# Performance work log

Hardware: AMD Instinct MI355X
Metric: run time of the kernel (lower is better)

## Reference

```python
import jax, jax.numpy as jnp
import numpy as np

DIM = 768
HEADS = 12
HEAD_DIM = DIM // HEADS
SCALE = HEAD_DIM ** (-0.5)


def setup_inputs() -> dict:
    key = jax.random.key(0)
    k1, k2, k3 = jax.random.split(key, 3)
    x = jax.random.normal(k1, (4, 2048, DIM), dtype=jnp.float32)
    # nn.Linear(dim, 3*dim, bias=False): weight [3*dim, dim]
    w_qkv = jax.random.normal(k2, (3 * DIM, DIM), dtype=jnp.float32) * (DIM ** -0.5)
    # nn.Linear(dim, dim) with bias
    w_proj = jax.random.normal(k3, (DIM, DIM), dtype=jnp.float32) * (DIM ** -0.5)
    b_proj = jnp.zeros((DIM,), dtype=jnp.float32)
    return {"x": x, "w_qkv": w_qkv, "w_proj": w_proj, "b_proj": b_proj}


def reference(x, w_qkv, w_proj, b_proj):
    B, N, C = x.shape
    H, D = HEADS, HEAD_DIM
    qkv = jnp.einsum('bnc,oc->bno', x, w_qkv)  # [B,N,3C]
    qkv = qkv.reshape(B, N, 3, H, D).transpose(2, 0, 3, 1, 4)  # [3,B,H,N,D]
    q, k, v = qkv[0], qkv[1], qkv[2]
    attn = jnp.einsum('bhnd,bhmd->bhnm', q, k) * SCALE  # [B,H,N,N]
    attn = jax.nn.softmax(attn, axis=-1)
    attn = jax.nn.softmax(attn, axis=-1)  # double softmax, as in original
    out = jnp.einsum('bhnm,bhmd->bhnd', attn, v)  # [B,H,N,D]
    out = out.transpose(0, 2, 1, 3).reshape(B, N, C)
    return jnp.einsum('bnc,oc->bno', out, w_proj) + b_proj
```

## Files before the change

kernel.cpp:

```cpp
#include <hip/hip_runtime.h>
#include <hip/hip_bf16.h>

#define DIM 768
#define HEADS 12
#define HD 64
#define SEQ 2048
#define BATCH 4
#define BHN 48
#define TOK 8192

#if __has_builtin(__builtin_amdgcn_exp2f)
#define EXP2F __builtin_amdgcn_exp2f
#else
#define EXP2F exp2f
#endif
#define EXP_C 0.1803368801111244f

using short8  = __attribute__((ext_vector_type(8))) short;
using float4v = __attribute__((ext_vector_type(4))) float;

__device__ __forceinline__ short f2b(float f) {
    union { float f; unsigned u; } v; v.f = f;
    unsigned r = v.u + 0x7FFF + ((v.u >> 16) & 1);
    return (short)(r >> 16);
}
__device__ __forceinline__ float b2f(short s) {
    union { unsigned u; float f; } v;
    v.u = ((unsigned)(unsigned short)s) << 16;
    return v.f;
}
__device__ __forceinline__ unsigned pk2(float a, float b) {
    union { float f; unsigned u; } x, y; x.f = a; y.f = b;
    return ((x.u + 0x8000u) >> 16) | ((y.u + 0x8000u) & 0xFFFF0000u);
}

typedef const __attribute__((address_space(1))) unsigned GU;
typedef __attribute__((address_space(3))) unsigned LU;
__device__ __forceinline__ void gload_lds16(const short* g, short* l) {
    __builtin_amdgcn_global_load_lds((GU*)g, (LU*)l, 16, 0, 0);
}

__global__ void cast_all(const float* __restrict__ x, const float* __restrict__ wq,
                         const float* __restrict__ wp,
                         short* __restrict__ xb, short* __restrict__ wqb,
                         short* __restrict__ wpb, int nx4, int nq4) {
    int i = blockIdx.x * 256 + threadIdx.x;
    const float* in; short* out; int j = i;
    if (i < nx4)            { in = x;  out = xb;  }
    else if (i < nx4 + nq4) { in = wq; out = wqb; j = i - nx4; }
    else                    { in = wp; out = wpb; j = i - nx4 - nq4; }
    float4 f = ((const float4*)in)[j];
    short4 o;
    o.x = f2b(f.x); o.y = f2b(f.y); o.z = f2b(f.z); o.w = f2b(f.w);
    ((short4*)out)[j] = o;
}

__global__ void vsum_kernel(const short* __restrict__ Vw, float* __restrict__ Vsum) {
    int wid  = blockIdx.x * 4 + (threadIdx.x >> 6);
    int lane = threadIdx.x & 63;
    const short* row = Vw + (size_t)wid * SEQ;
    float s = 0.f;
    for (int i = lane; i < SEQ; i += 64) s += b2f(row[i]);
    #pragma unroll
    for (int m = 1; m < 64; m <<= 1) s += __shfl_xor(s, m, 64);
    if (lane == 0) Vsum[wid] = s;
}

template<int MODE>
__global__ __launch_bounds__(256, 4)
void gemm_bt(const short* __restrict__ A, const short* __restrict__ Bw,
             const float* __restrict__ bias,
             short* __restrict__ Qw, short* __restrict__ Kw, short* __restrict__ Vw,
             float* __restrict__ Out, int K)
{
    __shared__ __align__(16) short As[128 * 32];
    __shared__ __align__(16) short Bs[128 * 32];

    const int tid  = threadIdx.x;
    const int lane = tid & 63;
    const int wave = tid >> 6;
    const int wm = (wave >> 1) * 64, wn = (wave & 1) * 64;
    const int l15 = lane & 15, quad = lane >> 4;

    const bool vpart = (MODE == 0) && (blockIdx.x >= 12);
    const short* rowsP = vpart ? (Bw + 1536 * 768) : A;
    const short* colsP = vpart ? A : Bw;
    const int m0 = vpart ? (blockIdx.x - 12) * 128 : blockIdx.y * 128;
    const int n0 = vpart ? blockIdx.y * 128 : blockIdx.x * 128;

    float4v acc[4][4];
    #pragma unroll
    for (int i = 0; i < 4; i++)
        #pragma unroll
        for (int j = 0; j < 4; j++)
            acc[i][j] = (float4v){0.f, 0.f, 0.f, 0.f};

    const int G0 = wave * 128 + lane;
    const int G1 = G0 + 64;
    const int rA0 = G0 >> 2, cA0 = (G0 & 3) * 8;
    const int rA1 = G1 >> 2, cA1 = (G1 & 3) * 8;
    short* ldsA0 = &As[(wave * 128) * 8];
    short* ldsA1 = &As[(wave * 128 + 64) * 8];
    short* ldsB0 = &Bs[(wave * 128) * 8];
    short* ldsB1 = &Bs[(wave * 128 + 64) * 8];

    for (int kt = 0; kt < K; kt += 32) {
        gload_lds16(&rowsP[(size_t)(m0 + rA0) * K + kt + cA0], ldsA0);
        gload_lds16(&rowsP[(size_t)(m0 + rA1) * K + kt + cA1], ldsA1);
        gload_lds16(&colsP[(size_t)(n0 + rA0) * K + kt + cA0], ldsB0);
        gload_lds16(&colsP[(size_t)(n0 + rA1) * K + kt + cA1], ldsB1);
        __syncthreads();
        short8 af[4], bfr[4];
        #pragma unroll
        for (int t = 0; t < 4; t++) {
            af[t]  = *(const short8*)&As[(wm + t * 16 + l15) * 32 + quad * 8];
            bfr[t] = *(const short8*)&Bs[(wn + t * 16 + l15) * 32 + quad * 8];
        }
        #pragma unroll
        for (int tm = 0; tm < 4; tm++)
            #pragma unroll
            for (int tn = 0; tn < 4; tn++)
                acc[tm][tn] = __builtin_amdgcn_mfma_f32_16x16x32_bf16(af[tm], bfr[tn], acc[tm][tn], 0, 0, 0);
        __syncthreads();
    }

    #pragma unroll
    for (int tm = 0; tm < 4; tm++)
        #pragma unroll
        for (int tn = 0; tn < 4; tn++)
            #pragma unroll
            for (int r = 0; r < 4; r++) {
                int row = m0 + wm + tm * 16 + quad * 4 + r;
                int col = n0 + wn + tn * 16 + l15;
                float v = acc[tm][tn][r];
                if (MODE == 0) {
                    if (vpart) {
                        int hh = row >> 6, d = row & 63;
                        int b = col >> 11, n = col & 2047;
                        Vw[((size_t)(b * HEADS + hh) * 64 + d) * SEQ + n] = f2b(v);
                    } else {
                        int hh = (col & 767) >> 6, d = col & 63;
                        int b = row >> 11, n = row & 2047;
                        int bh = b * HEADS + hh;
                        if (col < 768) Qw[((size_t)bh * SEQ + n) * 64 + d] = f2b(v * EXP_C);
                        else           Kw[((size_t)bh * SEQ + n) * 64 + d] = f2b(v);
                    }
                } else {
                    Out[(size_t)row * 768 + col] = v + bias[col];
                }
            }
}

__global__ __launch_bounds__(256, 3)
void attn_kernel(const short* __restrict__ Qw, const short* __restrict__ Kw,
                 const short* __restrict__ Vw, const float* __restrict__ Vsum,
                 short* __restrict__ Ow)
{
    __shared__ __align__(16) short KE[128 * 72];
    __shared__ __align__(16) short Eb[64 * 136];
    __shared__ __align__(16) short Vt[64 * 136];

    const int tid  = threadIdx.x;
    const int lane = tid & 63, wave = tid >> 6;
    const int l15 = lane & 15, quad = lane >> 4;
    const int bh = blockIdx.x >> 5;
    const int n0 = (blockIdx.x & 31) * 64;
    const int wq = (wave & 2) * 16;
    const int wk = (wave & 1) * 64;

    const short* Qp = Qw + (size_t)bh * SEQ * 64;
    const short* Kp = Kw + (size_t)bh * SEQ * 64;
    const short* Vp = Vw + (size_t)bh * 64 * SEQ;

    short8 onesf;
    #pragma unroll
    for (int j = 0; j < 8; j++) onesf[j] = (l15 == 0) ? (short)0x3F80 : (short)0;

    #pragma unroll
    for (int h = 0; h < 2; h++) {
        int c = tid + h * 256;
        int row = c >> 3, cc = (c & 7) * 8;
        *(short8*)&Eb[row * 72 + cc] = *(const short8*)&Qp[(size_t)(n0 + row) * 64 + cc];
    }
    __syncthreads();
    short8 aq[2][2];
    #pragma unroll
    for (int nb = 0; nb < 2; nb++)
        #pragma unroll
        for (int kk = 0; kk < 2; kk++)
            aq[nb][kk] = *(const short8*)&Eb[(wq + nb * 16 + l15) * 72 + kk * 32 + quad * 8];

    float4v Aacc[2][4], Lacc[2];
    #pragma unroll
    for (int mb = 0; mb < 2; mb++) {
        Lacc[mb] = (float4v){0.f, 0.f, 0.f, 0.f};
        #pragma unroll
        for (int t = 0; t < 4; t++) Aacc[mb][t] = (float4v){0.f, 0.f, 0.f, 0.f};
    }

    short8 kr[4], vr[4];
    #pragma unroll
    for (int h = 0; h < 4; h++) {
        int c = tid + h * 256;
        int row = c >> 3, cc = (c & 7) * 8;
        kr[h] = *(const short8*)&Kp[(size_t)row * 64 + cc];
        int vrow = c >> 4, vc = (c & 15) * 8;
        vr[h] = *(const short8*)&Vp[(size_t)vrow * SEQ + vc];
    }

    for (int kt = 0; kt < 16; kt++) {
        __syncthreads();
        #pragma unroll
        for (int h = 0; h < 4; h++) {
            int c = tid + h * 256;
            int row = c >> 3, cc = (c & 7) * 8;
            *(short8*)&KE[row * 72 + cc] = kr[h];
            int vrow = c >> 4, vc = (c & 15) * 8;
            *(short8*)&Vt[vrow * 136 + vc] = vr[h];
        }
        __syncthreads();

        if (kt < 15) {
            #pragma unroll
            for (int h = 0; h < 4; h++) {
                int c = tid + h * 256;
                int row = c >> 3, cc = (c & 7) * 8;
                kr[h] = *(const short8*)&Kp[(size_t)((kt + 1) * 128 + row) * 64 + cc];
                int vrow = c >> 4, vc = (c & 15) * 8;
                vr[h] = *(const short8*)&Vp[(size_t)vrow * SEQ + (kt + 1) * 128 + vc];
            }
        }

        float4v sacc[2][4];
        #pragma unroll
        for (int nb = 0; nb < 2; nb++)
            #pragma unroll
            for (int tn = 0; tn < 4; tn++) sacc[nb][tn] = (float4v){0.f, 0.f, 0.f, 0.f};
        #pragma unroll
        for (int tn = 0; tn < 4; tn++) {
            const int rowK = (wk + tn * 16 + l15) * 72;
            short8 b0 = *(const short8*)&KE[rowK + quad * 8];
            short8 b1 = *(const short8*)&KE[rowK + 32 + quad * 8];
            #pragma unroll
            for (int nb = 0; nb < 2; nb++) {
                sacc[nb][tn] = __builtin_amdgcn_mfma_f32_16x16x32_bf16(b0, aq[nb][0], sacc[nb][tn], 0, 0, 0);
                sacc[nb][tn] = __builtin_amdgcn_mfma_f32_16x16x32_bf16(b1, aq[nb][1], sacc[nb][tn], 0, 0, 0);
            }
        }

        #pragma unroll
        for (int nb = 0; nb < 2; nb++) {
            const int qrow = (wq + nb * 16 + l15) * 136;
            #pragma unroll
            for (int tn = 0; tn < 4; tn++) {
                float e0 = EXP2F(sacc[nb][tn][0]);
                float e1 = EXP2F(sacc[nb][tn][1]);
                float e2 = EXP2F(sacc[nb][tn][2]);
                float e3 = EXP2F(sacc[nb][tn][3]);
                uint2 u; u.x = pk2(e0, e1); u.y = pk2(e2, e3);
                *(uint2*)&Eb[qrow + wk + tn * 16 + quad * 4] = u;
            }
        }

        #pragma unroll
        for (int ks = 0; ks < 2; ks++) {
            const int koff = wk + ks * 32 + quad * 8;
            short8 ae0 = *(const short8*)&Eb[(wq + l15) * 136 + koff];
            short8 ae1 = *(const short8*)&Eb[(wq + 16 + l15) * 136 + koff];
            Lacc[0] = __builtin_amdgcn_mfma_f32_16x16x32_bf16(ae0, onesf, Lacc[0], 0, 0, 0);
            Lacc[1] = __builtin_amdgcn_mfma_f32_16x16x32_bf16(ae1, onesf, Lacc[1], 0, 0, 0);
            #pragma unroll
            for (int tn = 0; tn < 4; tn++) {
                short8 bv = *(const short8*)&Vt[(tn * 16 + l15) * 136 + koff];
                Aacc[0][tn] = __builtin_amdgcn_mfma_f32_16x16x32_bf16(ae0, bv, Aacc[0][tn], 0, 0, 0);
                Aacc[1][tn] = __builtin_amdgcn_mfma_f32_16x16x32_bf16(ae1, bv, Aacc[1][tn], 0, 0, 0);
            }
        }
    }

    __syncthreads();
    float* KEf = (float*)KE;
    float* Vtf = (float*)Vt;
    const int p = wave >> 1;
    if (wave & 1) {
        #pragma unroll
        for (int mb = 0; mb < 2; mb++) {
            #pragma unroll
            for (int tn = 0; tn < 4; tn++)
                #pragma unroll
                for (int r = 0; r < 4; r++)
                    KEf[(mb * 16 + tn * 4 + r) * 128 + p * 64 + lane] = Aacc[mb][tn][r];
            #pragma unroll
            for (int r = 0; r < 4; r++)
                Vtf[(mb * 4 + r) * 128 + p * 64 + lane] = Lacc[mb][r];
        }
    }
    __syncthreads();
    if (!(wave & 1)) {
        float il[2][4];
        #pragma unroll
        for (int mb = 0; mb < 2; mb++)
            #pragma unroll
            for (int r = 0; r < 4; r++) {
                float ls = Lacc[mb][r] + Vtf[(mb * 4 + r) * 128 + p * 64 + lane];
                il[mb][r] = 1.f / __shfl(ls, lane & 48, 64);
            }
        const int b = bh / HEADS, hh = bh - (bh / HEADS) * HEADS;
        #pragma unroll
        for (int tn = 0; tn < 4; tn++) {
            int d = tn * 16 + l15;
            float vs = Vsum[bh * 64 + d];
            #pragma unroll
            for (int mb = 0; mb < 2; mb++)
                #pragma unroll
                for (int r = 0; r < 4; r++) {
                    float a = Aacc[mb][tn][r] + KEf[(mb * 16 + tn * 4 + r) * 128 + p * 64 + lane];
                    int row = n0 + wq + mb * 16 + quad * 4 + r;
                    float val = (vs + a * il[mb][r]) * (1.f / 2049.f);
                    int tok = b * SEQ + row;
                    Ow[(size_t)tok * 768 + hh * 64 + d] = f2b(val);
                }
        }
    }
}

extern "C" void kernel_launch(void* const* d_in, const int* in_sizes, int n_in,
                              void* d_out, int out_size, void* d_ws, size_t ws_size,
                              hipStream_t stream) {
    const float* x      = (const float*)d_in[0];
    const float* w_qkv  = (const float*)d_in[1];
    const float* w_proj = (const float*)d_in[2];
    const float* b_proj = (const float*)d_in[3];
    float* out = (float*)d_out;

    char* ws = (char*)d_ws;
    size_t off = 0;
    auto alloc = [&](size_t bytes) {
        void* p = ws + off;
        off += (bytes + 255) & ~(size_t)255;
        return p;
    };
    short* x_bf  = (short*)alloc((size_t)TOK * DIM * 2);
    short* wq_bf = (short*)alloc((size_t)3 * DIM * DIM * 2);
    short* wp_bf = (short*)alloc((size_t)DIM * DIM * 2);
    short* Qw    = (short*)alloc((size_t)BHN * SEQ * 64 * 2);
    short* Kw    = (short*)alloc((size_t)BHN * SEQ * 64 * 2);
    short* Vw    = (short*)alloc((size_t)BHN * SEQ * 64 * 2);
    short* Ow    = (short*)alloc((size_t)TOK * DIM * 2);
    float* Vsum  = (float*)alloc((size_t)BHN * 64 * 4);

    int nx4 = TOK * DIM / 4, nq4 = 3 * DIM * DIM / 4, np4 = DIM * DIM / 4;
    int tot4 = nx4 + nq4 + np4;
    cast_all<<<tot4 / 256, 256, 0, stream>>>(x, w_qkv, w_proj, x_bf, wq_bf, wp_bf, nx4, nq4);

    dim3 g1(18, TOK / 128);
    gemm_bt<0><<<g1, 256, 0, stream>>>(x_bf, wq_bf, nullptr, Qw, Kw, Vw, nullptr, DIM);

    vsum_kernel<<<BHN * 64 / 4, 256, 0, stream>>>(Vw, Vsum);

    attn_kernel<<<BHN * 32, 256, 0, stream>>>(Qw, Kw, Vw, Vsum, Ow);

    dim3 g3(DIM / 128, TOK / 128);
    gemm_bt<1><<<g3, 256, 0, stream>>>(Ow, wp_bf, b_proj, nullptr, nullptr, nullptr, out, DIM);
}
```

Before: 243.2 us.

## Split GEMM into QKV and projection kernels with grouped block order and K=64 stages

The templated GEMM becomes two kernels. Each one now loads two 32-wide K slices per barrier pair, which halves the number of __syncthreads calls, and maps a 1D grid through grouped swizzling so neighbouring blocks share A/B tiles in L2. The projection GEMM switches to 128x64 tiles, giving 768 blocks instead of 384 so the GPU's CUs are filled better. The cost is twice the LDS per block, which may limit occupancy, and still no overlap of the loads with the MFMA work.

Result: faster. 226.0 us (-7.1%).

```diff
diff --git a/kernel.cpp b/kernel.cpp
--- a/kernel.cpp
+++ b/kernel.cpp
@@ -66,15 +66,12 @@
     if (lane == 0) Vsum[wid] = s;
 }
 
-template<int MODE>
 __global__ __launch_bounds__(256, 4)
-void gemm_bt(const short* __restrict__ A, const short* __restrict__ Bw,
-             const float* __restrict__ bias,
-             short* __restrict__ Qw, short* __restrict__ Kw, short* __restrict__ Vw,
-             float* __restrict__ Out, int K)
+void gemm_qkv(const short* __restrict__ A, const short* __restrict__ Bw,
+              short* __restrict__ Qw, short* __restrict__ Kw, short* __restrict__ Vw)
 {
-    __shared__ __align__(16) short As[128 * 32];
-    __shared__ __align__(16) short Bs[128 * 32];
+    __shared__ __align__(16) short As[2][128 * 32];
+    __shared__ __align__(16) short Bs[2][128 * 32];
 
     const int tid  = threadIdx.x;
     const int lane = tid & 63;
@@ -82,11 +79,17 @@
     const int wm = (wave >> 1) * 64, wn = (wave & 1) * 64;
     const int l15 = lane & 15, quad = lane >> 4;
 
-    const bool vpart = (MODE == 0) && (blockIdx.x >= 12);
+    const int gid = blockIdx.x;
+    const int w   = gid >> 3;
+    const int ybl = (gid & 7) * 8 + (w & 7);
+    const int xbl = w >> 3;
+
+    const bool vpart = (xbl >= 12);
     const short* rowsP = vpart ? (Bw + 1536 * 768) : A;
     const short* colsP = vpart ? A : Bw;
-    const int m0 = vpart ? (blockIdx.x - 12) * 128 : blockIdx.y * 128;
-    const int n0 = vpart ? blockIdx.y * 128 : blockIdx.x * 128;
+    const int m0 = vpart ? (xbl - 12) * 128 : ybl * 128;
+    const int n0 = vpart ? ybl * 128 : xbl * 128;
+    const int K = DIM;
 
     float4v acc[4][4];
     #pragma unroll
@@ -99,28 +102,32 @@
     const int G1 = G0 + 64;
     const int rA0 = G0 >> 2, cA0 = (G0 & 3) * 8;
     const int rA1 = G1 >> 2, cA1 = (G1 & 3) * 8;
-    short* ldsA0 = &As[(wave * 128) * 8];
-    short* ldsA1 = &As[(wave * 128 + 64) * 8];
-    short* ldsB0 = &Bs[(wave * 128) * 8];
-    short* ldsB1 = &Bs[(wave * 128 + 64) * 8];
-
-    for (int kt = 0; kt < K; kt += 32) {
-        gload_lds16(&rowsP[(size_t)(m0 + rA0) * K + kt + cA0], ldsA0);
-        gload_lds16(&rowsP[(size_t)(m0 + rA1) * K + kt + cA1], ldsA1);
-        gload_lds16(&colsP[(size_t)(n0 + rA0) * K + kt + cA0], ldsB0);
-        gload_lds16(&colsP[(size_t)(n0 + rA1) * K + kt + cA1], ldsB1);
-        __syncthreads();
-        short8 af[4], bfr[4];
-        #pragma unroll
-        for (int t = 0; t < 4; t++) {
-            af[t]  = *(const short8*)&As[(wm + t * 16 + l15) * 32 + quad * 8];
-            bfr[t] = *(const short8*)&Bs[(wn + t * 16 + l15) * 32 + quad * 8];
-        }
-        #pragma unroll
-        for (int tm = 0; tm < 4; tm++)
-            #pragma unroll
-            for (int tn = 0; tn < 4; tn++)
-                acc[tm][tn] = __builtin_amdgcn_mfma_f32_16x16x32_bf16(af[tm], bfr[tn], acc[tm][tn], 0, 0, 0);
+    const int ldsoff = wave * 1024;
+
+    for (int kt = 0; kt < K; kt += 64) {
+        #pragma unroll
+        for (int s = 0; s < 2; s++) {
+            const int kc = kt + s * 32;
+            gload_lds16(&rowsP[(size_t)(m0 + rA0) * K + kc + cA0], &As[s][ldsoff]);
+            gload_lds16(&rowsP[(size_t)(m0 + rA1) * K + kc + cA1], &As[s][ldsoff + 512]);
+            gload_lds16(&colsP[(size_t)(n0 + rA0) * K + kc + cA0], &Bs[s][ldsoff]);
+            gload_lds16(&colsP[(size_t)(n0 + rA1) * K + kc + cA1], &Bs[s][ldsoff + 512]);
+        }
+        __syncthreads();
+        #pragma unroll
+        for (int s = 0; s < 2; s++) {
+            short8 af[4], bfr[4];
+            #pragma unroll
+            for (int t = 0; t < 4; t++) {
+                af[t]  = *(const short8*)&As[s][(wm + t * 16 + l15) * 32 + quad * 8];
+                bfr[t] = *(const short8*)&Bs[s][(wn + t * 16 + l15) * 32 + quad * 8];
+            }
+            #pragma unroll
+            for (int tm = 0; tm < 4; tm++)
+                #pragma unroll
+                for (int tn = 0; tn < 4; tn++)
+                    acc[tm][tn] = __builtin_amdgcn_mfma_f32_16x16x32_bf16(af[tm], bfr[tn], acc[tm][tn], 0, 0, 0);
+        }
         __syncthreads();
     }
 
@@ -133,21 +140,90 @@
                 int row = m0 + wm + tm * 16 + quad * 4 + r;
                 int col = n0 + wn + tn * 16 + l15;
                 float v = acc[tm][tn][r];
-                if (MODE == 0) {
-                    if (vpart) {
-                        int hh = row >> 6, d = row & 63;
-                        int b = col >> 11, n = col & 2047;
-                        Vw[((size_t)(b * HEADS + hh) * 64 + d) * SEQ + n] = f2b(v);
-                    } else {
-                        int hh = (col & 767) >> 6, d = col & 63;
-                        int b = row >> 11, n = row & 2047;
-                        int bh = b * HEADS + hh;
-                        if (col < 768) Qw[((size_t)bh * SEQ + n) * 64 + d] = f2b(v * EXP_C);
-                        else           Kw[((size_t)bh * SEQ + n) * 64 + d] = f2b(v);
-                    }
+                if (vpart) {
+                    int hh = row >> 6, d = row & 63;
+                    int b = col >> 11, n = col & 2047;
+                    Vw[((size_t)(b * HEADS + hh) * 64 + d) * SEQ + n] = f2b(v);
                 } else {
-                    Out[(size_t)row * 768 + col] = v + bias[col];
+                    int hh = (col & 767) >> 6, d = col & 63;
+                    int b = row >> 11, n = row & 2047;
+                    int bh = b * HEADS + hh;
+                    if (col < 768) Qw[((size_t)bh * SEQ + n) * 64 + d] = f2b(v * EXP_C);
+                    else           Kw[((size_t)bh * SEQ + n) * 64 + d] = f2b(v);
                 }
+            }
+}
+
+__global__ __launch_bounds__(256, 4)
+void gemm_proj(const short* __restrict__ A, const short* __restrict__ Bw,
+               const float* __restrict__ bias, float* __restrict__ Out)
+{
+    __shared__ __align__(16) short As[2][128 * 32];
+    __shared__ __align__(16) short Bs[2][64 * 32];
+
+    const int tid  = threadIdx.x;
+    const int lane = tid & 63;
+    const int wave = tid >> 6;
+    const int wm = (wave >> 1) * 64, wn = (wave & 1) * 32;
+    const int l15 = lane & 15, quad = lane >> 4;
+
+    const int gid = blockIdx.x;
+    const int w   = gid >> 3;
+    const int ybl = (gid & 7) * 8 + (w & 7);
+    const int xbl = w >> 3;
+    const int m0 = ybl * 128, n0 = xbl * 64;
+    const int K = DIM;
+
+    float4v acc[4][2];
+    #pragma unroll
+    for (int i = 0; i < 4; i++)
+        #pragma unroll
+        for (int j = 0; j < 2; j++)
+            acc[i][j] = (float4v){0.f, 0.f, 0.f, 0.f};
+
+    const int GA0 = wave * 128 + lane, GA1 = GA0 + 64;
+    const int rA0 = GA0 >> 2, cA0 = (GA0 & 3) * 8;
+    const int rA1 = GA1 >> 2, cA1 = (GA1 & 3) * 8;
+    const int GB0 = wave * 64 + lane;
+    const int rB0 = GB0 >> 2, cB0 = (GB0 & 3) * 8;
+    const int ldsoffA = wave * 1024, ldsoffB = wave * 512;
+
+    for (int kt = 0; kt < K; kt += 64) {
+        #pragma unroll
+        for (int s = 0; s < 2; s++) {
+            const int kc = kt + s * 32;
+            gload_lds16(&A [(size_t)(m0 + rA0) * K + kc + cA0], &As[s][ldsoffA]);
+            gload_lds16(&A [(size_t)(m0 + rA1) * K + kc + cA1], &As[s][ldsoffA + 512]);
+            gload_lds16(&Bw[(size_t)(n0 + rB0) * K + kc + cB0], &Bs[s][ldsoffB]);
+        }
+        __syncthreads();
+        #pragma unroll
+        for (int s = 0; s < 2; s++) {
+            short8 af[4], bfr[2];
+            #pragma unroll
+            for (int t = 0; t < 4; t++)
+                af[t] = *(const short8*)&As[s][(wm + t * 16 + l15) * 32 + quad * 8];
+            #pragma unroll
+            for (int t = 0; t < 2; t++)
+                bfr[t] = *(const short8*)&Bs[s][(wn + t * 16 + l15) * 32 + quad * 8];
+            #pragma unroll
+            for (int tm = 0; tm < 4; tm++)
+                #pragma unroll
+                for (int tn = 0; tn < 2; tn++)
+                    acc[tm][tn] = __builtin_amdgcn_mfma_f32_16x16x32_bf16(af[tm], bfr[tn], acc[tm][tn], 0, 0, 0);
+        }
+        __syncthreads();
+    }
+
+    #pragma unroll
+    for (int tm = 0; tm < 4; tm++)
+        #pragma unroll
+        for (int tn = 0; tn < 2; tn++)
+            #pragma unroll
+            for (int r = 0; r < 4; r++) {
+                int row = m0 + wm + tm * 16 + quad * 4 + r;
+                int col = n0 + wn + tn * 16 + l15;
+                Out[(size_t)row * 768 + col] = acc[tm][tn][r] + bias[col];
             }
 }
 
@@ -353,13 +429,11 @@
     int tot4 = nx4 + nq4 + np4;
     cast_all<<<tot4 / 256, 256, 0, stream>>>(x, w_qkv, w_proj, x_bf, wq_bf, wp_bf, nx4, nq4);
 
-    dim3 g1(18, TOK / 128);
-    gemm_bt<0><<<g1, 256, 0, stream>>>(x_bf, wq_bf, nullptr, Qw, Kw, Vw, nullptr, DIM);
+    gemm_qkv<<<1152, 256, 0, stream>>>(x_bf, wq_bf, Qw, Kw, Vw);
 
     vsum_kernel<<<BHN * 64 / 4, 256, 0, stream>>>(Vw, Vsum);
 
     attn_kernel<<<BHN * 32, 256, 0, stream>>>(Qw, Kw, Vw, Vsum, Ow);
 
-    dim3 g3(DIM / 128, TOK / 128);
-    gemm_bt<1><<<g3, 256, 0, stream>>>(Ow, wp_bf, b_proj, nullptr, nullptr, nullptr, out, DIM);
-}
+    gemm_proj<<<768, 256, 0, stream>>>(Ow, wp_bf, b_proj, out);
+}
```
